# Kernel optimization log

Measured on AMD Instinct MI355X. Metric: run time of the kernel, lower is better.

Reference implementation:

```python
import jax, jax.numpy as jnp
import numpy as np

IN_C, HID_C, OUT_C = 602, 256, 41
N_SRC0, N_TGT0, N_TGT1 = 256000, 10240, 1024
E0, E1 = 256000, 10240


def setup_inputs() -> dict:
    key = jax.random.key(0)
    ks = jax.random.split(key, 12)
    x = jax.random.normal(ks[0], (N_SRC0, IN_C), dtype=jnp.float32)
    src0 = jax.random.randint(ks[1], (E0,), 0, N_SRC0, dtype=jnp.int32)
    dst0 = jax.random.randint(ks[2], (E0,), 0, N_TGT0, dtype=jnp.int32)
    src1 = jax.random.randint(ks[3], (E1,), 0, N_TGT0, dtype=jnp.int32)
    dst1 = jax.random.randint(ks[4], (E1,), 0, N_TGT1, dtype=jnp.int32)
    s1 = 1.0 / np.sqrt(IN_C)
    s2 = 1.0 / np.sqrt(HID_C)
    Wl1 = jax.random.uniform(ks[5], (IN_C, HID_C), jnp.float32, -s1, s1)
    Wr1 = jax.random.uniform(ks[6], (IN_C, HID_C), jnp.float32, -s1, s1)
    b1 = jnp.zeros((HID_C,), jnp.float32)
    Wl2 = jax.random.uniform(ks[7], (HID_C, OUT_C), jnp.float32, -s2, s2)
    Wr2 = jax.random.uniform(ks[8], (HID_C, OUT_C), jnp.float32, -s2, s2)
    b2 = jnp.zeros((OUT_C,), jnp.float32)
    return {"x": x, "src0": src0, "dst0": dst0, "src1": src1, "dst1": dst1,
            "Wl1": Wl1, "Wr1": Wr1, "b1": b1, "Wl2": Wl2, "Wr2": Wr2, "b2": b2,
            "n_tgt0": N_TGT0, "n_tgt1": N_TGT1}


def _sage_conv(x_src, x_tgt, src, dst, Wl, Wr, b, n_tgt):
    # mean aggregation of source messages per target node (0 for isolated targets)
    msg = x_src[src]                                                   # [E, C]
    ssum = jax.ops.segment_sum(msg, dst, num_segments=n_tgt)           # [n_tgt, C]
    cnt = jax.ops.segment_sum(jnp.ones((src.shape[0], 1), x_src.dtype), dst,
                              num_segments=n_tgt)
    agg = ssum / jnp.maximum(cnt, 1.0)
    return agg @ Wl + x_tgt @ Wr + b


def reference(x, src0, dst0, src1, dst1, Wl1, Wr1, b1, Wl2, Wr2, b2, n_tgt0, n_tgt1):
    # layer 1: bipartite SAGEConv, x_target = x[:n_tgt0]
    h = _sage_conv(x, x[:n_tgt0], src0, dst0, Wl1, Wr1, b1, n_tgt0)
    h = jax.nn.relu(h)  # dropout omitted (eval / deterministic)
    # layer 2
    out = _sage_conv(h, h[:n_tgt1], src1, dst1, Wl2, Wr2, b2, n_tgt1)
    return jax.nn.log_softmax(out, axis=-1)
```

## Files before the change

kernel.cpp:

```cpp
#include <hip/hip_runtime.h>
#include <hip/hip_bf16.h>

#define IN_C   602
#define HID_C  256
#define OUT_C  41
#define N_TGT0 10240
#define N_TGT1 1024
#define E0     256000
#define E1     10240
#define KTOT   1216
#define NWK    (HID_C * KTOT)

typedef unsigned short u16;
typedef __attribute__((ext_vector_type(4))) float f32x4;
typedef __attribute__((ext_vector_type(8))) short bf16x8;

__device__ __forceinline__ u16 f2bf(float v) {
    union { float f; unsigned u; } c; c.f = v;
    unsigned u = c.u;
    u += 0x7fffu + ((u >> 16) & 1u);
    return (u16)(u >> 16);
}
__device__ __forceinline__ float bf2f(u16 v) {
    union { unsigned u; float f; } c; c.u = ((unsigned)v) << 16; return c.f;
}

__device__ __forceinline__ void gload16(const void* g, void* l) {
    __builtin_amdgcn_global_load_lds(
        (const __attribute__((address_space(1))) void*)g,
        (__attribute__((address_space(3))) void*)l, 16, 0, 0);
}

__global__ __launch_bounds__(256) void build_kernel(
    const int* __restrict__ src0, const int* __restrict__ dst0,
    const int* __restrict__ src1, const int* __restrict__ dst1,
    int* __restrict__ head0, int* __restrict__ next0,
    int* __restrict__ head1, int* __restrict__ next1,
    const float* __restrict__ Wl, const float* __restrict__ Wr, u16* __restrict__ BT)
{
    int id = blockIdx.x * 256 + threadIdx.x;
    if (id < E0) {
        int p = atomicExch(&head0[dst0[id]], id);
        next0[id] = p;
    } else if (id < E0 + E1) {
        int e = id - E0;
        int p = atomicExch(&head1[dst1[e]], e);
        next1[e] = p;
    }
    if (id < NWK) {
        int n = id / KTOT, k = id - n * KTOT;
        float v = 0.f;
        if (k < IN_C)                        v = Wl[(size_t)k * HID_C + n];
        else if (k >= 608 && k < 608 + IN_C) v = Wr[(size_t)(k - 608) * HID_C + n];
        BT[id] = f2bf(v);
    }
}

__global__ __launch_bounds__(256) void agg0_ll(
    const float* __restrict__ x, const int* __restrict__ head,
    const int* __restrict__ next, const int* __restrict__ srcv,
    u16* __restrict__ A)
{
    int t = blockIdx.x * 4 + (threadIdx.x >> 6);
    int lane = threadIdx.x & 63;

    float2 a0 = make_float2(0.f, 0.f), a1 = a0, a2 = a0, a3 = a0, a4 = a0;
    int d = 0;

    int cur = head[t];
    int s   = (cur >= 0) ? srcv[cur] : 0;
    int nxt = (cur >= 0) ? next[cur] : -1;
    while (cur >= 0) {
        const float2* r = (const float2*)(x + (size_t)s * IN_C);
        float2 v0 = r[lane], v1 = r[lane + 64], v2 = r[lane + 128], v3 = r[lane + 192];
        int curN = nxt;
        int sN   = (curN >= 0) ? srcv[curN] : 0;
        int nxtN = (curN >= 0) ? next[curN] : -1;
        a0.x += v0.x; a0.y += v0.y;
        a1.x += v1.x; a1.y += v1.y;
        a2.x += v2.x; a2.y += v2.y;
        a3.x += v3.x; a3.y += v3.y;
        if (lane < 45) {
            float2 v4 = r[lane + 256];
            a4.x += v4.x; a4.y += v4.y;
        }
        ++d;
        cur = curN; s = sN; nxt = nxtN;
    }

    float inv = 1.0f / (float)(d > 1 ? d : 1);
    ushort2* orow = (ushort2*)(A + (size_t)t * KTOT);
    ushort2 o;
    o.x = f2bf(a0.x * inv); o.y = f2bf(a0.y * inv); orow[lane]       = o;
    o.x = f2bf(a1.x * inv); o.y = f2bf(a1.y * inv); orow[lane + 64]  = o;
    o.x = f2bf(a2.x * inv); o.y = f2bf(a2.y * inv); orow[lane + 128] = o;
    o.x = f2bf(a3.x * inv); o.y = f2bf(a3.y * inv); orow[lane + 192] = o;
    if (lane < 45) {
        o.x = f2bf(a4.x * inv); o.y = f2bf(a4.y * inv); orow[lane + 256] = o;
    } else if (lane < 48) {
        o.x = 0; o.y = 0; orow[lane + 256] = o;
    }

    const float2* xt = (const float2*)(x + (size_t)t * IN_C);
    ushort2* orow2 = orow + 304;
    float2 w0 = xt[lane], w1 = xt[lane + 64], w2 = xt[lane + 128], w3 = xt[lane + 192];
    o.x = f2bf(w0.x); o.y = f2bf(w0.y); orow2[lane]       = o;
    o.x = f2bf(w1.x); o.y = f2bf(w1.y); orow2[lane + 64]  = o;
    o.x = f2bf(w2.x); o.y = f2bf(w2.y); orow2[lane + 128] = o;
    o.x = f2bf(w3.x); o.y = f2bf(w3.y); orow2[lane + 192] = o;
    if (lane < 45) {
        float2 w4 = xt[lane + 256];
        o.x = f2bf(w4.x); o.y = f2bf(w4.y); orow2[lane + 256] = o;
    } else if (lane < 48) {
        o.x = 0; o.y = 0; orow2[lane + 256] = o;
    }
}

#define GBM 64
#define GBN 64
#define GBK 64
#define GNIT (KTOT / GBK)

__global__ __launch_bounds__(256) void gemm1_tile(
    const u16* __restrict__ A, const u16* __restrict__ BT,
    const float* __restrict__ bias, u16* __restrict__ h)
{
    __shared__ __align__(16) u16 As[2][GBM * GBK];
    __shared__ __align__(16) u16 Bs[2][GBN * GBK];
    int tid = threadIdx.x;
    int w = tid >> 6, lane = tid & 63;
    int d = blockIdx.x;
    int ni = (d >> 3) & 3;
    int mi = (d & 7) + ((d >> 5) << 3);
    int bm = mi * GBM, bn = ni * GBN;

    int r16 = lane & 15;
    int g = lane >> 4;
    int wm2 = w >> 1, wn2 = w & 1;

    int srow = lane >> 3;
    int sslot = (lane & 7) ^ srow;
    const u16* gA0 = A  + (size_t)(bm + w * 16 + srow) * KTOT + sslot * 8;
    const u16* gA1 = gA0 + (size_t)8 * KTOT;
    const u16* gB0 = BT + (size_t)(bn + w * 16 + srow) * KTOT + sslot * 8;
    const u16* gB1 = gB0 + (size_t)8 * KTOT;

    int xr = r16 & 7;
    int rowA0 = wm2 * 32 + r16;
    int rowB0 = wn2 * 32 + r16;

    f32x4 acc[2][2] = {};

    auto stage = [&](int buf, int k0) {
        u16* dA = &As[buf][w * 1024];
        u16* dB = &Bs[buf][w * 1024];
        gload16(gA0 + k0, dA);
        gload16(gA1 + k0, dA + 512);
        gload16(gB0 + k0, dB);
        gload16(gB1 + k0, dB + 512);
    };

    stage(0, 0);
    stage(1, GBK);
    asm volatile("s_waitcnt vmcnt(4)" ::: "memory");
    __builtin_amdgcn_sched_barrier(0);
    __builtin_amdgcn_s_barrier();

    int cur = 0;
    for (int it = 0; it < GNIT; ++it) {
        #pragma unroll
        for (int ks = 0; ks < 2; ++ks) {
            int sl = ((ks << 2) + g);
            bf16x8 a0 = *(const bf16x8*)(&As[cur][rowA0 * 64 + ((sl ^ xr) << 3)]);
            bf16x8 a1 = *(const bf16x8*)(&As[cur][(rowA0 + 16) * 64 + ((sl ^ xr) << 3)]);
            bf16x8 b0 = *(const bf16x8*)(&Bs[cur][rowB0 * 64 + ((sl ^ xr) << 3)]);
            bf16x8 b1 = *(const bf16x8*)(&Bs[cur][(rowB0 + 16) * 64 + ((sl ^ xr) << 3)]);
            acc[0][0] = __builtin_amdgcn_mfma_f32_16x16x32_bf16(a0, b0, acc[0][0], 0, 0, 0);
            acc[0][1] = __builtin_amdgcn_mfma_f32_16x16x32_bf16(a0, b1, acc[0][1], 0, 0, 0);
            acc[1][0] = __builtin_amdgcn_mfma_f32_16x16x32_bf16(a1, b0, acc[1][0], 0, 0, 0);
            acc[1][1] = __builtin_amdgcn_mfma_f32_16x16x32_bf16(a1, b1, acc[1][1], 0, 0, 0);
        }

        if (it + 1 < GNIT) {
            asm volatile("s_waitcnt lgkmcnt(0)" ::: "memory");
            __builtin_amdgcn_sched_barrier(0);
            __builtin_amdgcn_s_barrier();
            if (it + 2 < GNIT) {
                stage(cur, (it + 2) * GBK);
                asm volatile("s_waitcnt vmcnt(4)" ::: "memory");
            } else {
                asm volatile("s_waitcnt vmcnt(0)" ::: "memory");
            }
            __builtin_amdgcn_sched_barrier(0);
            __builtin_amdgcn_s_barrier();
            cur ^= 1;
        }
    }

    int row4 = g * 4;
    #pragma unroll
    for (int fn = 0; fn < 2; ++fn) {
        int n = bn + wn2 * 32 + fn * 16 + r16;
        float b = bias[n];
        #pragma unroll
        for (int fm = 0; fm < 2; ++fm) {
            #pragma unroll
            for (int j = 0; j < 4; ++j) {
                int m = bm + wm2 * 32 + fm * 16 + row4 + j;
                float v = acc[fm][fn][j] + b;
                h[(size_t)m * HID_C + n] = f2bf(v > 0.f ? v : 0.f);
            }
        }
    }
}

__global__ __launch_bounds__(64) void out_fused(
    const u16* __restrict__ h, const int* __restrict__ head,
    const int* __restrict__ next, const int* __restrict__ srcv,
    const float* __restrict__ Wl, const float* __restrict__ Wr,
    const float* __restrict__ bias, float* __restrict__ out)
{
    __shared__ float arow[HID_C];
    __shared__ float hrow[HID_C];
    int t = blockIdx.x;
    int lane = threadIdx.x;

    float4 acc = make_float4(0.f, 0.f, 0.f, 0.f);
    int d = 0;
    int cur = head[t];
    int s   = (cur >= 0) ? srcv[cur] : 0;
    int nxt = (cur >= 0) ? next[cur] : -1;
    while (cur >= 0) {
        ushort4 v = ((const ushort4*)(h + (size_t)s * HID_C))[lane];
        int curN = nxt;
        int sN   = (curN >= 0) ? srcv[curN] : 0;
        int nxtN = (curN >= 0) ? next[curN] : -1;
        acc.x += bf2f(v.x); acc.y += bf2f(v.y);
        acc.z += bf2f(v.z); acc.w += bf2f(v.w);
        ++d;
        cur = curN; s = sN; nxt = nxtN;
    }
    float inv = 1.0f / (float)(d > 1 ? d : 1);
    ((float4*)arow)[lane] = make_float4(acc.x * inv, acc.y * inv, acc.z * inv, acc.w * inv);
    ushort4 hv = ((const ushort4*)(h + (size_t)t * HID_C))[lane];
    ((float4*)hrow)[lane] = make_float4(bf2f(hv.x), bf2f(hv.y), bf2f(hv.z), bf2f(hv.w));
    __syncthreads();

    float v = 0.f;
    if (lane < OUT_C) {
        v = bias[lane];
        for (int k = 0; k < HID_C; ++k)
            v += arow[k] * Wl[k * OUT_C + lane] + hrow[k] * Wr[k * OUT_C + lane];
    }
    float m = (lane < OUT_C) ? v : -1e30f;
    #pragma unroll
    for (int off = 32; off; off >>= 1) m = fmaxf(m, __shfl_xor(m, off));
    float ex = (lane < OUT_C) ? expf(v - m) : 0.f;
    float sum = ex;
    #pragma unroll
    for (int off = 32; off; off >>= 1) sum += __shfl_xor(sum, off);
    float lse = m + logf(sum);
    if (lane < OUT_C) out[(size_t)t * OUT_C + lane] = v - lse;
}


extern "C" void kernel_launch(void* const* d_in, const int* in_sizes, int n_in,
                              void* d_out, int out_size, void* d_ws, size_t ws_size,
                              hipStream_t stream) {
    const float* x    = (const float*)d_in[0];
    const int*   src0 = (const int*)d_in[1];
    const int*   dst0 = (const int*)d_in[2];
    const int*   src1 = (const int*)d_in[3];
    const int*   dst1 = (const int*)d_in[4];
    const float* Wl1  = (const float*)d_in[5];
    const float* Wr1  = (const float*)d_in[6];
    const float* b1   = (const float*)d_in[7];
    const float* Wl2  = (const float*)d_in[8];
    const float* Wr2  = (const float*)d_in[9];
    const float* b2   = (const float*)d_in[10];
    float* out = (float*)d_out;

    char* ws = (char*)d_ws;
    size_t off = 0;
    auto take = [&](size_t bytes) { void* p = ws + off; off += (bytes + 255) & ~(size_t)255; return p; };
    u16* A     = (u16*)take((size_t)N_TGT0 * KTOT * 2);
    u16* BT    = (u16*)take((size_t)HID_C * KTOT * 2);
    u16* h     = (u16*)take((size_t)N_TGT0 * HID_C * 2);
    int* head0 = (int*)take((size_t)(N_TGT0 + N_TGT1) * 4);
    int* head1 = head0 + N_TGT0;
    int* next0 = (int*)take((size_t)E0 * 4);
    int* next1 = (int*)take((size_t)E1 * 4);

    hipMemsetAsync(head0, 0xFF, (size_t)(N_TGT0 + N_TGT1) * sizeof(int), stream);

    build_kernel<<<(NWK + 255) / 256, 256, 0, stream>>>(
        src0, dst0, src1, dst1, head0, next0, head1, next1, Wl1, Wr1, BT);

    agg0_ll<<<N_TGT0 / 4, 256, 0, stream>>>(x, head0, next0, src0, A);

    gemm1_tile<<<640, 256, 0, stream>>>(A, BT, b1, h);

    out_fused<<<N_TGT1, 64, 0, stream>>>(h, head1, next1, src1, Wl2, Wr2, b2, out);
}
```

Measured before the change: 180.3 us.

## Collect neighbor indices in registers then gather rows four at a time

The layer-1 aggregation kernel now walks the linked list first and stashes up to 128 source indices in lane registers, without loading feature rows during the walk. It then loads those rows four at a time with 16-byte vector loads, so many independent row gathers are in flight together instead of being serialized behind the pointer chase. Row loads and output stores move from float2 to float4/ushort4 granularity. Targets with more than 128 neighbors fall back to accumulating inline, and the change adds register pressure and shuffle overhead.

```diff
diff --git a/kernel.cpp b/kernel.cpp
--- a/kernel.cpp
+++ b/kernel.cpp
@@ -23,6 +23,15 @@
 }
 __device__ __forceinline__ float bf2f(u16 v) {
     union { unsigned u; float f; } c; c.u = ((unsigned)v) << 16; return c.f;
+}
+__device__ __forceinline__ f32x4 ld4(const float* p) {
+    f32x4 v; __builtin_memcpy(&v, p, 16); return v;
+}
+__device__ __forceinline__ ushort4 pack4(f32x4 v, float inv) {
+    ushort4 o;
+    o.x = f2bf(v.x * inv); o.y = f2bf(v.y * inv);
+    o.z = f2bf(v.z * inv); o.w = f2bf(v.w * inv);
+    return o;
 }
 
 __device__ __forceinline__ void gload16(const void* g, void* l) {
@@ -56,63 +65,103 @@
     }
 }
 
-__global__ __launch_bounds__(256) void agg0_ll(
+__global__ __launch_bounds__(256) void agg0_reg(
     const float* __restrict__ x, const int* __restrict__ head,
     const int* __restrict__ next, const int* __restrict__ srcv,
     u16* __restrict__ A)
 {
     int t = blockIdx.x * 4 + (threadIdx.x >> 6);
     int lane = threadIdx.x & 63;
-
-    float2 a0 = make_float2(0.f, 0.f), a1 = a0, a2 = a0, a3 = a0, a4 = a0;
+    int l4 = lane * 4;
+
+    f32x4 a0 = {0.f, 0.f, 0.f, 0.f}, a1 = a0, a2 = a0;
+    float tx = 0.f, ty = 0.f;
     int d = 0;
+    int my0 = 0, my1 = 0;
 
     int cur = head[t];
     int s   = (cur >= 0) ? srcv[cur] : 0;
     int nxt = (cur >= 0) ? next[cur] : -1;
     while (cur >= 0) {
-        const float2* r = (const float2*)(x + (size_t)s * IN_C);
-        float2 v0 = r[lane], v1 = r[lane + 64], v2 = r[lane + 128], v3 = r[lane + 192];
         int curN = nxt;
         int sN   = (curN >= 0) ? srcv[curN] : 0;
         int nxtN = (curN >= 0) ? next[curN] : -1;
-        a0.x += v0.x; a0.y += v0.y;
-        a1.x += v1.x; a1.y += v1.y;
-        a2.x += v2.x; a2.y += v2.y;
-        a3.x += v3.x; a3.y += v3.y;
-        if (lane < 45) {
-            float2 v4 = r[lane + 256];
-            a4.x += v4.x; a4.y += v4.y;
+        if (d < 64) {
+            if (lane == d) my0 = s;
+        } else if (d < 128) {
+            if (lane == d - 64) my1 = s;
+        } else {
+            const float* p = x + (size_t)s * IN_C;
+            a0 += ld4(p + l4);
+            a1 += ld4(p + 256 + l4);
+            if (lane < 22) a2 += ld4(p + 512 + l4);
+            else if (lane == 22) { float2 v = *(const float2*)(p + 600); tx += v.x; ty += v.y; }
         }
         ++d;
         cur = curN; s = sN; nxt = nxtN;
     }
 
+    int dcap = d < 128 ? d : 128;
+    int j = 0;
+    for (; j + 3 < dcap; j += 4) {
+        int s0 = __shfl((j + 0 < 64) ? my0 : my1, (j + 0) & 63);
+        int s1 = __shfl((j + 1 < 64) ? my0 : my1, (j + 1) & 63);
+        int s2 = __shfl((j + 2 < 64) ? my0 : my1, (j + 2) & 63);
+        int s3 = __shfl((j + 3 < 64) ? my0 : my1, (j + 3) & 63);
+        const float* p0 = x + (size_t)s0 * IN_C;
+        const float* p1 = x + (size_t)s1 * IN_C;
+        const float* p2 = x + (size_t)s2 * IN_C;
+        const float* p3 = x + (size_t)s3 * IN_C;
+        f32x4 A0 = ld4(p0 + l4),       B0 = ld4(p1 + l4),       C0 = ld4(p2 + l4),       D0 = ld4(p3 + l4);
+        f32x4 A1 = ld4(p0 + 256 + l4), B1 = ld4(p1 + 256 + l4), C1 = ld4(p2 + 256 + l4), D1 = ld4(p3 + 256 + l4);
+        a0 += (A0 + B0) + (C0 + D0);
+        a1 += (A1 + B1) + (C1 + D1);
+        if (lane < 22) {
+            f32x4 A2 = ld4(p0 + 512 + l4), B2 = ld4(p1 + 512 + l4);
+            f32x4 C2 = ld4(p2 + 512 + l4), D2 = ld4(p3 + 512 + l4);
+            a2 += (A2 + B2) + (C2 + D2);
+        } else if (lane == 22) {
+            float2 v0 = *(const float2*)(p0 + 600), v1 = *(const float2*)(p1 + 600);
+            float2 v2 = *(const float2*)(p2 + 600), v3 = *(const float2*)(p3 + 600);
+            tx += (v0.x + v1.x) + (v2.x + v3.x);
+            ty += (v0.y + v1.y) + (v2.y + v3.y);
+        }
+    }
+    for (; j < dcap; ++j) {
+        int sj = __shfl((j < 64) ? my0 : my1, j & 63);
+        const float* p = x + (size_t)sj * IN_C;
+        a0 += ld4(p + l4);
+        a1 += ld4(p + 256 + l4);
+        if (lane < 22) a2 += ld4(p + 512 + l4);
+        else if (lane == 22) { float2 v = *(const float2*)(p + 600); tx += v.x; ty += v.y; }
+    }
+
     float inv = 1.0f / (float)(d > 1 ? d : 1);
-    ushort2* orow = (ushort2*)(A + (size_t)t * KTOT);
-    ushort2 o;
-    o.x = f2bf(a0.x * inv); o.y = f2bf(a0.y * inv); orow[lane]       = o;
-    o.x = f2bf(a1.x * inv); o.y = f2bf(a1.y * inv); orow[lane + 64]  = o;
-    o.x = f2bf(a2.x * inv); o.y = f2bf(a2.y * inv); orow[lane + 128] = o;
-    o.x = f2bf(a3.x * inv); o.y = f2bf(a3.y * inv); orow[lane + 192] = o;
-    if (lane < 45) {
-        o.x = f2bf(a4.x * inv); o.y = f2bf(a4.y * inv); orow[lane + 256] = o;
-    } else if (lane < 48) {
-        o.x = 0; o.y = 0; orow[lane + 256] = o;
-    }
-
-    const float2* xt = (const float2*)(x + (size_t)t * IN_C);
-    ushort2* orow2 = orow + 304;
-    float2 w0 = xt[lane], w1 = xt[lane + 64], w2 = xt[lane + 128], w3 = xt[lane + 192];
-    o.x = f2bf(w0.x); o.y = f2bf(w0.y); orow2[lane]       = o;
-    o.x = f2bf(w1.x); o.y = f2bf(w1.y); orow2[lane + 64]  = o;
-    o.x = f2bf(w2.x); o.y = f2bf(w2.y); orow2[lane + 128] = o;
-    o.x = f2bf(w3.x); o.y = f2bf(w3.y); orow2[lane + 192] = o;
-    if (lane < 45) {
-        float2 w4 = xt[lane + 256];
-        o.x = f2bf(w4.x); o.y = f2bf(w4.y); orow2[lane + 256] = o;
-    } else if (lane < 48) {
-        o.x = 0; o.y = 0; orow2[lane + 256] = o;
+    ushort4* orow = (ushort4*)(A + (size_t)t * KTOT);
+    orow[lane]      = pack4(a0, inv);
+    orow[64 + lane] = pack4(a1, inv);
+    if (lane < 22) {
+        orow[128 + lane] = pack4(a2, inv);
+    } else if (lane == 22) {
+        ushort4 o; o.x = f2bf(tx * inv); o.y = f2bf(ty * inv); o.z = 0; o.w = 0;
+        orow[150] = o;
+    } else if (lane == 23) {
+        orow[151] = make_ushort4(0, 0, 0, 0);
+    }
+
+    const float* xt = x + (size_t)t * IN_C;
+    f32x4 w0 = ld4(xt + l4);
+    f32x4 w1 = ld4(xt + 256 + l4);
+    orow[152 + lane]      = pack4(w0, 1.0f);
+    orow[152 + 64 + lane] = pack4(w1, 1.0f);
+    if (lane < 22) {
+        orow[152 + 128 + lane] = pack4(ld4(xt + 512 + l4), 1.0f);
+    } else if (lane == 22) {
+        float2 v = *(const float2*)(xt + 600);
+        ushort4 o; o.x = f2bf(v.x); o.y = f2bf(v.y); o.z = 0; o.w = 0;
+        orow[152 + 150] = o;
+    } else if (lane == 23) {
+        orow[152 + 151] = make_ushort4(0, 0, 0, 0);
     }
 }
 
@@ -296,7 +345,7 @@
     build_kernel<<<(NWK + 255) / 256, 256, 0, stream>>>(
         src0, dst0, src1, dst1, head0, next0, head1, next1, Wl1, Wr1, BT);
 
-    agg0_ll<<<N_TGT0 / 4, 256, 0, stream>>>(x, head0, next0, src0, A);
+    agg0_reg<<<N_TGT0 / 4, 256, 0, stream>>>(x, head0, next0, src0, A);
 
     gemm1_tile<<<640, 256, 0, stream>>>(A, BT, b1, h);
 
```

Measured after the change: 188.8 us. +4.7%, slower.
